# Kernel optimization log

Measured on AMD Instinct MI355X. Metric: run time of the kernel, lower is better.

The kernel has to match this reference:

```python
import jax, jax.numpy as jnp
import numpy as np


def setup_inputs() -> dict:
    key = jax.random.key(0)
    k1, k2, k3, k4 = jax.random.split(key, 4)
    B, S, T = 128, 512, 256
    return {
        "emissions": jax.random.normal(k1, (B, S, T), dtype=jnp.float32),
        "mask": jnp.ones((B, S), dtype=bool),
        "start_transitions": jax.random.normal(k2, (T,), dtype=jnp.float32),
        "end_transitions": jax.random.normal(k3, (T,), dtype=jnp.float32),
        "transitions": jax.random.normal(k4, (T, T), dtype=jnp.float32),
    }


def reference(emissions, mask, start_transitions, end_transitions, transitions):
    # emissions: [B, S, T], mask: [B, S] bool, transitions: [T, T]
    init = start_transitions[None, :] + emissions[:, 0]  # [B, T]
    em_t = jnp.swapaxes(emissions[:, 1:], 0, 1)  # [S-1, B, T] time-major
    mk_t = jnp.swapaxes(mask[:, 1:], 0, 1)       # [S-1, B]

    def lse_step(state, em):
        # state[b, i] + transitions[i, j] + em[b, j] -> logsumexp over i
        inner = state[:, :, None] + transitions[None, :, :] + em[:, None, :]
        return jax.nn.logsumexp(inner, axis=1)

    # _compute_score: mask-aware logsumexp recurrence (as written in the module)
    def step_score(score, xs):
        em, mk = xs
        nxt = lse_step(score, em)
        return jnp.where(mk[:, None], nxt, score), None

    score, _ = jax.lax.scan(step_score, init, (em_t, mk_t))
    score = jax.nn.logsumexp(score + end_transitions[None, :], axis=1)  # [B]

    # _compute_partition: same recurrence, mask where() is a no-op in the source
    def step_part(alpha, em):
        return lse_step(alpha, em), None

    alpha, _ = jax.lax.scan(step_part, init, em_t)
    partition = jax.nn.logsumexp(alpha + end_transitions[None, :], axis=1)  # [B]

    return partition - score
```

## Files before the change

kernel.cpp:

```cpp
#include <hip/hip_runtime.h>
#include <hip/hip_bf16.h>
#include <stdint.h>

#define LOG2E 1.44269504088896340736f
#define LN2   0.69314718055994530942f

typedef __attribute__((ext_vector_type(8))) __bf16 bf16x8;
typedef __attribute__((ext_vector_type(4))) float  f32x4;

static constexpr int B = 128, S = 512, T = 256;
static constexpr int LDP = T + 8;
static constexpr int H   = 260;
static constexpr int NSF = H;
static constexpr int NSB = S - 1 - H;

static __device__ __forceinline__ uint pack_bf16x2(float a, float b) {
    __hip_bfloat162 h = __float22bfloat162_rn(make_float2(a, b));
    union { __hip_bfloat162 h; uint u; } cv; cv.h = h;
    return cv.u;
}
static __device__ __forceinline__ float bf2f(ushort u) {
    return __uint_as_float(((uint)u) << 16);
}

static __device__ __forceinline__ void wg_barrier() {
    asm volatile("s_waitcnt lgkmcnt(0)" ::: "memory");
    __builtin_amdgcn_s_barrier();
    __builtin_amdgcn_sched_barrier(0);
}

static __device__ __forceinline__ float vmax44(const float v[4][4]) {
    float m = 0.0f;
    #pragma unroll
    for (int t = 0; t < 4; ++t)
        #pragma unroll
        for (int r = 0; r < 4; ++r) m = fmaxf(m, v[t][r]);
    return m;
}

__global__ void prep_mats(const float* __restrict__ trans,
                          ushort* __restrict__ Et, ushort* __restrict__ Em) {
    int i = blockIdx.x;
    int j = threadIdx.x;
    float e = exp2f(trans[i * T + j] * LOG2E);
    uint u = __float_as_uint(e);
    ushort h = (ushort)((u + 0x7FFFu + ((u >> 16) & 1u)) >> 16);
    Em[i * T + j] = h;
    Et[j * T + i] = h;
}

__global__ void prep_emx(const float* __restrict__ em, ushort* __restrict__ emx) {
    size_t i4 = ((size_t)blockIdx.x * blockDim.x + threadIdx.x) * 4;
    f32x4 e = *reinterpret_cast<const f32x4*>(&em[i4]);
    uint2 w;
    w.x = pack_bf16x2(exp2f(e[0] * LOG2E), exp2f(e[1] * LOG2E));
    w.y = pack_bf16x2(exp2f(e[2] * LOG2E), exp2f(e[3] * LOG2E));
    *reinterpret_cast<uint2*>(&emx[i4]) = w;
}

template<bool PRE, int DIR>
static __device__ __forceinline__ void scan_body(
    const float* __restrict__ em, const ushort* __restrict__ emx,
    const int* __restrict__ mask, const float* __restrict__ startt,
    const float* __restrict__ endt, const ushort* __restrict__ Amat,
    float* __restrict__ vecbuf, int* __restrict__ lsbuf,
    const int scan, const int b,
    ushort (&Al)[2][16][LDP], float (&mx2)[16][4])
{
    constexpr int NSTEP = DIR ? NSB : NSF;
    constexpr int PGRP  = (NSTEP + 7) / 8;

    const int tid  = threadIdx.x;
    const int jq   = tid >> 6;
    const int lane = tid & 63;
    const int q    = lane >> 4;
    const int l    = lane & 15;

    #define EROW(ix) (DIR ? (S - 2 - (ix)) : (1 + (ix)))
    #define MROW(ix) (DIR ? (S - 1 - (ix)) : (1 + (ix)))

    bf16x8 Afr[4][8];
    #pragma unroll
    for (int mt = 0; mt < 4; ++mt) {
        int j = jq * 64 + mt * 16 + l;
        #pragma unroll
        for (int kt = 0; kt < 8; ++kt)
            Afr[mt][kt] = *reinterpret_cast<const bf16x8*>(&Amat[j * T + kt * 32 + q * 8]);
    }

    const float*  emrow = em  + (size_t)b * S * T;
    const ushort* exrow = PRE ? emx + (size_t)b * S * T : nullptr;
    const int*    mrow  = mask + (size_t)b * S;

    int ls = 0;
    int buf = 0;
    float areg[4][4];

    {
        const int    r0 = DIR ? (S - 1) : 0;
        const float* tv = DIR ? endt : startt;
        float v0[4][4], gg[4][4]; float mx = 0.0f;
        #pragma unroll
        for (int t = 0; t < 4; ++t) {
            int j0 = jq * 64 + t * 16 + q * 4;
            f32x4 e4 = *reinterpret_cast<const f32x4*>(&emrow[(size_t)r0 * T + j0]);
            f32x4 s4 = *reinterpret_cast<const f32x4*>(&tv[j0]);
            #pragma unroll
            for (int r = 0; r < 4; ++r) {
                float full = exp2f((e4[r] + s4[r]) * LOG2E);
                v0[t][r] = full;
                gg[t][r] = DIR ? exp2f(s4[r] * LOG2E) : full;
                mx = fmaxf(mx, full);
            }
        }
        mx = fmaxf(mx, __shfl_xor(mx, 16));
        mx = fmaxf(mx, __shfl_xor(mx, 32));
        if (q == 0) mx2[l][jq] = mx;
        __syncthreads();
        f32x4 m4 = *reinterpret_cast<const f32x4*>(&mx2[l][0]);
        float gmx = fmaxf(fmaxf(m4[0], m4[1]), fmaxf(m4[2], m4[3]));
        int e = (int)((__float_as_uint(gmx) >> 23) & 255u) - 127;
        float sc = __uint_as_float((uint)(127 - e) << 23);
        ls = e;
        #pragma unroll
        for (int t = 0; t < 4; ++t) {
            int j0 = jq * 64 + t * 16 + q * 4;
            uint2 w;
            w.x = pack_bf16x2(v0[t][0] * sc, v0[t][1] * sc);
            w.y = pack_bf16x2(v0[t][2] * sc, v0[t][3] * sc);
            *reinterpret_cast<uint2*>(&Al[0][l][j0]) = w;
            if (DIR) {
                #pragma unroll
                for (int r = 0; r < 4; ++r) areg[t][r] = gg[t][r] * sc;
            }
        }
        __syncthreads();
        if (q == 0) mx2[l][jq] = mx * sc;
        __syncthreads();
    }

    const bool track = (DIR == 0) && (scan != 0);

    uint2 exv[8][4]; int mks[8];
    #pragma unroll
    for (int u = 0; u < 8; ++u) {
        int iu = u < NSTEP ? u : NSTEP - 1;
        #pragma unroll
        for (int t = 0; t < 4; ++t) {
            int j0 = jq * 64 + t * 16 + q * 4;
            if (PRE) exv[u][t] = *reinterpret_cast<const uint2*>(&exrow[(size_t)EROW(iu) * T + j0]);
        }
        mks[u] = (scan && u < NSTEP) ? mrow[MROW(u)] : 1;
    }

    for (int p = 0; p < PGRP; ++p) {
        uint2 exn[8][4]; int mkn[8];
        #pragma unroll
        for (int u = 0; u < 8; ++u) {
            int idx  = 8 * (p + 1) + u;
            int idxc = idx < NSTEP ? idx : NSTEP - 1;
            #pragma unroll
            for (int t = 0; t < 4; ++t) {
                int j0 = jq * 64 + t * 16 + q * 4;
                if (PRE) exn[u][t] = *reinterpret_cast<const uint2*>(&exrow[(size_t)EROW(idxc) * T + j0]);
            }
            mkn[u] = (scan && idx < NSTEP) ? mrow[MROW(idxc)] : 1;
        }

        float pend = 1.0f, vml = 0.0f; int pk = 0;

        #pragma unroll
        for (int u = 0; u < 8; ++u) {
            const int idx = 8 * p + u;
            if (idx < NSTEP) {
                if ((u & 3) == 0) {
                    f32x4 m4 = *reinterpret_cast<const f32x4*>(&mx2[l][0]);
                    float gmx = fmaxf(fmaxf(m4[0], m4[1]), fmaxf(m4[2], m4[3]));
                    int kap = (int)((__float_as_uint(gmx) >> 23) & 255u) - 127;
                    pend = __uint_as_float((uint)(127 - kap) << 23);
                    pk   = kap;
                    vml  = gmx;
                }
                const int nb = buf ^ 1;

                bf16x8 bfr[8];
                #pragma unroll
                for (int kt = 0; kt < 8; ++kt)
                    bfr[kt] = *reinterpret_cast<const bf16x8*>(&Al[buf][l][kt * 32 + q * 8]);

                f32x4 acc[4] = {f32x4{0,0,0,0}, f32x4{0,0,0,0}, f32x4{0,0,0,0}, f32x4{0,0,0,0}};
                #pragma unroll
                for (int kt = 0; kt < 8; ++kt) {
                    #pragma unroll
                    for (int mt = 0; mt < 4; ++mt)
                        acc[mt] = __builtin_amdgcn_mfma_f32_16x16x32_bf16(Afr[mt][kt], bfr[kt], acc[mt], 0, 0, 0);
                }

                const int mk = mks[u];
                float v[4][4];

                #pragma unroll
                for (int t = 0; t < 4; ++t) {
                    float e_[4];
                    if (PRE) {
                        e_[0] = bf2f((ushort)(exv[u][t].x & 0xFFFF));
                        e_[1] = bf2f((ushort)(exv[u][t].x >> 16));
                        e_[2] = bf2f((ushort)(exv[u][t].y & 0xFFFF));
                        e_[3] = bf2f((ushort)(exv[u][t].y >> 16));
                    } else {
                        int j0 = jq * 64 + t * 16 + q * 4;
                        f32x4 e4 = *reinterpret_cast<const f32x4*>(&emrow[(size_t)EROW(idx) * T + j0]);
                        #pragma unroll
                        for (int r = 0; r < 4; ++r) e_[r] = exp2f(e4[r] * LOG2E);
                    }
                    if (DIR == 0) {
                        #pragma unroll
                        for (int r = 0; r < 4; ++r)
                            v[t][r] = acc[t][r] * e_[r] * pend;
                    } else {
                        #pragma unroll
                        for (int r = 0; r < 4; ++r) {
                            float g  = acc[t][r] * pend;
                            float sv = mk ? g : areg[t][r];
                            areg[t][r] = sv;
                            v[t][r] = sv * e_[r];
                        }
                    }
                }

                if (DIR == 0) {
                    if (mk) {
                        #pragma unroll
                        for (int t = 0; t < 4; ++t) {
                            int j0 = jq * 64 + t * 16 + q * 4;
                            uint2 w;
                            w.x = pack_bf16x2(v[t][0], v[t][1]);
                            w.y = pack_bf16x2(v[t][2], v[t][3]);
                            *reinterpret_cast<uint2*>(&Al[nb][l][j0]) = w;
                        }
                    } else {
                        #pragma unroll
                        for (int t = 0; t < 4; ++t) {
                            int j0 = jq * 64 + t * 16 + q * 4;
                            *reinterpret_cast<uint2*>(&Al[nb][l][j0]) =
                                *reinterpret_cast<const uint2*>(&Al[buf][l][j0]);
                        }
                    }
                } else {
                    #pragma unroll
                    for (int t = 0; t < 4; ++t) {
                        int j0 = jq * 64 + t * 16 + q * 4;
                        uint2 w;
                        w.x = pack_bf16x2(v[t][0], v[t][1]);
                        w.y = pack_bf16x2(v[t][2], v[t][3]);
                        *reinterpret_cast<uint2*>(&Al[nb][l][j0]) = w;
                    }
                }

                if (track) {
                    float lmx = vmax44(v);
                    vml = mk ? lmx : vml;
                }
                ls  += mk ? pk : 0;
                pend = mk ? 1.0f : pend;
                pk   = mk ? 0 : pk;

                const bool rn = ((u & 3) == 3) || (idx == NSTEP - 1);
                if (rn) {
                    float fm = track ? vml : vmax44(v);
                    fm = fmaxf(fm, __shfl_xor(fm, 16));
                    fm = fmaxf(fm, __shfl_xor(fm, 32));
                    if (q == 0) mx2[l][jq] = fm;
                }

                wg_barrier();
                buf = nb;
            }
        }

        #pragma unroll
        for (int u = 0; u < 8; ++u) {
            #pragma unroll
            for (int t = 0; t < 4; ++t) exv[u][t] = exn[u][t];
            mks[u] = mkn[u];
        }
    }

    const int cidx = scan * 2 + DIR;
    if (DIR) {
        #pragma unroll
        for (int t = 0; t < 4; ++t) {
            int j0 = jq * 64 + t * 16 + q * 4;
            f32x4 o = {areg[t][0], areg[t][1], areg[t][2], areg[t][3]};
            *reinterpret_cast<f32x4*>(&vecbuf[((size_t)cidx * B + b) * T + j0]) = o;
        }
    } else {
        #pragma unroll
        for (int t = 0; t < 4; ++t) {
            int j0 = jq * 64 + t * 16 + q * 4;
            uint2 w = *reinterpret_cast<const uint2*>(&Al[buf][l][j0]);
            f32x4 o = {bf2f((ushort)(w.x & 0xFFFF)), bf2f((ushort)(w.x >> 16)),
                       bf2f((ushort)(w.y & 0xFFFF)), bf2f((ushort)(w.y >> 16))};
            *reinterpret_cast<f32x4*>(&vecbuf[((size_t)cidx * B + b) * T + j0]) = o;
        }
    }
    if (jq == 0 && q == 0) lsbuf[cidx * B + b] = ls;

    #undef EROW
    #undef MROW
}

template<bool PRE>
__launch_bounds__(256, 1)
__global__ void crf_scan(const float* __restrict__ em,
                         const ushort* __restrict__ emx,
                         const int* __restrict__ mask,
                         const float* __restrict__ startt,
                         const float* __restrict__ endt,
                         const ushort* __restrict__ Et,
                         const ushort* __restrict__ Emat,
                         float* __restrict__ vecbuf,
                         int* __restrict__ lsbuf)
{
    __shared__ __align__(16) ushort Al[2][16][LDP];
    __shared__ __align__(16) float mx2[16][4];

    const int scan = blockIdx.x & 1;
    const int dir  = (blockIdx.x >> 1) & 1;
    const int bg   = blockIdx.x >> 2;
    const int b    = bg * 16 + (threadIdx.x & 15);

    if (dir == 0)
        scan_body<PRE, 0>(em, emx, mask, startt, endt, Et,   vecbuf, lsbuf, scan, b, Al, mx2);
    else
        scan_body<PRE, 1>(em, emx, mask, startt, endt, Emat, vecbuf, lsbuf, scan, b, Al, mx2);
}

__global__ void combine2(const float* __restrict__ vecbuf, const int* __restrict__ lsbuf,
                         float* __restrict__ out) {
    __shared__ float r2[2][B];
    int tid = threadIdx.x;
    int sc_ = tid >> 7, b = tid & 127;
    const float* vf = vecbuf + ((size_t)(sc_ * 2 + 0) * B + b) * T;
    const float* vb = vecbuf + ((size_t)(sc_ * 2 + 1) * B + b) * T;
    float dot = 0.0f;
    for (int j = 0; j < T; j += 4) {
        f32x4 a = *reinterpret_cast<const f32x4*>(&vf[j]);
        f32x4 c = *reinterpret_cast<const f32x4*>(&vb[j]);
        dot += a[0] * c[0] + a[1] * c[1] + a[2] * c[2] + a[3] * c[3];
    }
    r2[sc_][b] = (float)(lsbuf[(sc_ * 2) * B + b] + lsbuf[(sc_ * 2 + 1) * B + b]) + log2f(dot);
    __syncthreads();
    if (tid < B) out[tid] = (r2[0][tid] - r2[1][tid]) * LN2;
}

extern "C" void kernel_launch(void* const* d_in, const int* in_sizes, int n_in,
                              void* d_out, int out_size, void* d_ws, size_t ws_size,
                              hipStream_t stream) {
    (void)in_sizes; (void)n_in; (void)out_size;
    const float* em = (const float*)d_in[0];
    const int*   mk = (const int*)d_in[1];
    const float* st = (const float*)d_in[2];
    const float* en = (const float*)d_in[3];
    const float* tr = (const float*)d_in[4];

    const size_t emx_bytes = (size_t)B * S * T * sizeof(ushort);
    const size_t mat_bytes = (size_t)T * T * sizeof(ushort);
    const size_t vec_bytes = (size_t)4 * B * T * sizeof(float);
    const size_t ls_bytes  = (size_t)4 * B * sizeof(int);

    const bool pre = ws_size >= emx_bytes + 2 * mat_bytes + vec_bytes + ls_bytes;

    char* wp = (char*)d_ws;
    ushort* emx = nullptr;
    if (pre) { emx = (ushort*)wp; wp += emx_bytes; }
    ushort* Et = (ushort*)wp; wp += mat_bytes;
    ushort* Em = (ushort*)wp; wp += mat_bytes;
    float*  vec = (float*)wp; wp += vec_bytes;
    int*    lsb = (int*)wp;

    prep_mats<<<T, T, 0, stream>>>(tr, Et, Em);
    if (pre) {
        prep_emx<<<(B * S * T) / (256 * 4), 256, 0, stream>>>(em, emx);
        crf_scan<true><<<32, 256, 0, stream>>>(em, emx, mk, st, en, Et, Em, vec, lsb);
    } else {
        crf_scan<false><<<32, 256, 0, stream>>>(em, emx, mk, st, en, Et, Em, vec, lsb);
    }
    combine2<<<1, 256, 0, stream>>>(vec, lsb, (float*)d_out);
}
```

Baseline: 390.8 us.

## Split each scan block across eight waves with two MFMA tiles per wave

Each scan block now uses 512 threads, so eight waves each own 32 output tags instead of four waves owning 64. The per-step 256x256 matvec work per wave is halved, and the MFMA accumulation is split into two interleaved chains to shorten the dependency chain. The aim is to cut per-step latency on the serial recurrence. In exchange, the cross-wave max reduction now reads eight entries and the per-step barrier has to synchronise twice as many waves.

```diff
diff --git a/kernel.cpp b/kernel.cpp
--- a/kernel.cpp
+++ b/kernel.cpp
@@ -29,10 +29,10 @@
     __builtin_amdgcn_sched_barrier(0);
 }
 
-static __device__ __forceinline__ float vmax44(const float v[4][4]) {
+static __device__ __forceinline__ float vmax24(const float v[2][4]) {
     float m = 0.0f;
     #pragma unroll
-    for (int t = 0; t < 4; ++t)
+    for (int t = 0; t < 2; ++t)
         #pragma unroll
         for (int r = 0; r < 4; ++r) m = fmaxf(m, v[t][r]);
     return m;
@@ -64,28 +64,29 @@
     const int* __restrict__ mask, const float* __restrict__ startt,
     const float* __restrict__ endt, const ushort* __restrict__ Amat,
     float* __restrict__ vecbuf, int* __restrict__ lsbuf,
-    const int scan, const int b,
-    ushort (&Al)[2][16][LDP], float (&mx2)[16][4])
+    const int scan, const int bg,
+    ushort (&Al)[2][16][LDP], float (&mx2)[16][8])
 {
     constexpr int NSTEP = DIR ? NSB : NSF;
     constexpr int PGRP  = (NSTEP + 7) / 8;
 
     const int tid  = threadIdx.x;
-    const int jq   = tid >> 6;
+    const int w    = tid >> 6;
     const int lane = tid & 63;
     const int q    = lane >> 4;
     const int l    = lane & 15;
+    const int b    = bg * 16 + l;
 
     #define EROW(ix) (DIR ? (S - 2 - (ix)) : (1 + (ix)))
     #define MROW(ix) (DIR ? (S - 1 - (ix)) : (1 + (ix)))
 
-    bf16x8 Afr[4][8];
+    bf16x8 Afr[2][8];
     #pragma unroll
-    for (int mt = 0; mt < 4; ++mt) {
-        int j = jq * 64 + mt * 16 + l;
+    for (int t = 0; t < 2; ++t) {
+        int j = w * 32 + t * 16 + l;
         #pragma unroll
         for (int kt = 0; kt < 8; ++kt)
-            Afr[mt][kt] = *reinterpret_cast<const bf16x8*>(&Amat[j * T + kt * 32 + q * 8]);
+            Afr[t][kt] = *reinterpret_cast<const bf16x8*>(&Amat[j * T + kt * 32 + q * 8]);
     }
 
     const float*  emrow = em  + (size_t)b * S * T;
@@ -94,15 +95,15 @@
 
     int ls = 0;
     int buf = 0;
-    float areg[4][4];
+    float areg[2][4];
 
     {
         const int    r0 = DIR ? (S - 1) : 0;
         const float* tv = DIR ? endt : startt;
-        float v0[4][4], gg[4][4]; float mx = 0.0f;
-        #pragma unroll
-        for (int t = 0; t < 4; ++t) {
-            int j0 = jq * 64 + t * 16 + q * 4;
+        float v0[2][4], gg[2][4]; float mx = 0.0f;
+        #pragma unroll
+        for (int t = 0; t < 2; ++t) {
+            int j0 = w * 32 + t * 16 + q * 4;
             f32x4 e4 = *reinterpret_cast<const f32x4*>(&emrow[(size_t)r0 * T + j0]);
             f32x4 s4 = *reinterpret_cast<const f32x4*>(&tv[j0]);
             #pragma unroll
@@ -115,53 +116,55 @@
         }
         mx = fmaxf(mx, __shfl_xor(mx, 16));
         mx = fmaxf(mx, __shfl_xor(mx, 32));
-        if (q == 0) mx2[l][jq] = mx;
+        if (q == 0) mx2[l][w] = mx;
         __syncthreads();
-        f32x4 m4 = *reinterpret_cast<const f32x4*>(&mx2[l][0]);
-        float gmx = fmaxf(fmaxf(m4[0], m4[1]), fmaxf(m4[2], m4[3]));
+        f32x4 ma = *reinterpret_cast<const f32x4*>(&mx2[l][0]);
+        f32x4 mb = *reinterpret_cast<const f32x4*>(&mx2[l][4]);
+        float gmx = fmaxf(fmaxf(fmaxf(ma[0], ma[1]), fmaxf(ma[2], ma[3])),
+                          fmaxf(fmaxf(mb[0], mb[1]), fmaxf(mb[2], mb[3])));
         int e = (int)((__float_as_uint(gmx) >> 23) & 255u) - 127;
         float sc = __uint_as_float((uint)(127 - e) << 23);
         ls = e;
         #pragma unroll
-        for (int t = 0; t < 4; ++t) {
-            int j0 = jq * 64 + t * 16 + q * 4;
-            uint2 w;
-            w.x = pack_bf16x2(v0[t][0] * sc, v0[t][1] * sc);
-            w.y = pack_bf16x2(v0[t][2] * sc, v0[t][3] * sc);
-            *reinterpret_cast<uint2*>(&Al[0][l][j0]) = w;
+        for (int t = 0; t < 2; ++t) {
+            int j0 = w * 32 + t * 16 + q * 4;
+            uint2 wv;
+            wv.x = pack_bf16x2(v0[t][0] * sc, v0[t][1] * sc);
+            wv.y = pack_bf16x2(v0[t][2] * sc, v0[t][3] * sc);
+            *reinterpret_cast<uint2*>(&Al[0][l][j0]) = wv;
             if (DIR) {
                 #pragma unroll
                 for (int r = 0; r < 4; ++r) areg[t][r] = gg[t][r] * sc;
             }
         }
         __syncthreads();
-        if (q == 0) mx2[l][jq] = mx * sc;
+        if (q == 0) mx2[l][w] = mx * sc;
         __syncthreads();
     }
 
     const bool track = (DIR == 0) && (scan != 0);
 
-    uint2 exv[8][4]; int mks[8];
+    uint2 exv[8][2]; int mks[8];
     #pragma unroll
     for (int u = 0; u < 8; ++u) {
         int iu = u < NSTEP ? u : NSTEP - 1;
         #pragma unroll
-        for (int t = 0; t < 4; ++t) {
-            int j0 = jq * 64 + t * 16 + q * 4;
+        for (int t = 0; t < 2; ++t) {
+            int j0 = w * 32 + t * 16 + q * 4;
             if (PRE) exv[u][t] = *reinterpret_cast<const uint2*>(&exrow[(size_t)EROW(iu) * T + j0]);
         }
-        mks[u] = (scan && u < NSTEP) ? mrow[MROW(u)] : 1;
+        mks[u] = (scan && u < NSTEP) ? mrow[MROW(iu)] : 1;
     }
 
     for (int p = 0; p < PGRP; ++p) {
-        uint2 exn[8][4]; int mkn[8];
+        uint2 exn[8][2]; int mkn[8];
         #pragma unroll
         for (int u = 0; u < 8; ++u) {
             int idx  = 8 * (p + 1) + u;
             int idxc = idx < NSTEP ? idx : NSTEP - 1;
             #pragma unroll
-            for (int t = 0; t < 4; ++t) {
-                int j0 = jq * 64 + t * 16 + q * 4;
+            for (int t = 0; t < 2; ++t) {
+                int j0 = w * 32 + t * 16 + q * 4;
                 if (PRE) exn[u][t] = *reinterpret_cast<const uint2*>(&exrow[(size_t)EROW(idxc) * T + j0]);
             }
             mkn[u] = (scan && idx < NSTEP) ? mrow[MROW(idxc)] : 1;
@@ -174,8 +177,10 @@
             const int idx = 8 * p + u;
             if (idx < NSTEP) {
                 if ((u & 3) == 0) {
-                    f32x4 m4 = *reinterpret_cast<const f32x4*>(&mx2[l][0]);
-                    float gmx = fmaxf(fmaxf(m4[0], m4[1]), fmaxf(m4[2], m4[3]));
+                    f32x4 ma = *reinterpret_cast<const f32x4*>(&mx2[l][0]);
+                    f32x4 mb = *reinterpret_cast<const f32x4*>(&mx2[l][4]);
+                    float gmx = fmaxf(fmaxf(fmaxf(ma[0], ma[1]), fmaxf(ma[2], ma[3])),
+                                      fmaxf(fmaxf(mb[0], mb[1]), fmaxf(mb[2], mb[3])));
                     int kap = (int)((__float_as_uint(gmx) >> 23) & 255u) - 127;
                     pend = __uint_as_float((uint)(127 - kap) << 23);
                     pk   = kap;
@@ -188,19 +193,23 @@
                 for (int kt = 0; kt < 8; ++kt)
                     bfr[kt] = *reinterpret_cast<const bf16x8*>(&Al[buf][l][kt * 32 + q * 8]);
 
-                f32x4 acc[4] = {f32x4{0,0,0,0}, f32x4{0,0,0,0}, f32x4{0,0,0,0}, f32x4{0,0,0,0}};
+                f32x4 ac[2][2] = {{f32x4{0,0,0,0}, f32x4{0,0,0,0}},
+                                  {f32x4{0,0,0,0}, f32x4{0,0,0,0}}};
                 #pragma unroll
                 for (int kt = 0; kt < 8; ++kt) {
                     #pragma unroll
-                    for (int mt = 0; mt < 4; ++mt)
-                        acc[mt] = __builtin_amdgcn_mfma_f32_16x16x32_bf16(Afr[mt][kt], bfr[kt], acc[mt], 0, 0, 0);
-                }
+                    for (int t = 0; t < 2; ++t)
+                        ac[t][kt & 1] = __builtin_amdgcn_mfma_f32_16x16x32_bf16(Afr[t][kt], bfr[kt], ac[t][kt & 1], 0, 0, 0);
+                }
+                f32x4 acc[2];
+                #pragma unroll
+                for (int t = 0; t < 2; ++t) acc[t] = ac[t][0] + ac[t][1];
 
                 const int mk = mks[u];
-                float v[4][4];
-
-                #pragma unroll
-                for (int t = 0; t < 4; ++t) {
+                float v[2][4];
+
+                #pragma unroll
+                for (int t = 0; t < 2; ++t) {
                     float e_[4];
                     if (PRE) {
                         e_[0] = bf2f((ushort)(exv[u][t].x & 0xFFFF));
@@ -208,7 +217,7 @@
                         e_[2] = bf2f((ushort)(exv[u][t].y & 0xFFFF));
                         e_[3] = bf2f((ushort)(exv[u][t].y >> 16));
                     } else {
-                        int j0 = jq * 64 + t * 16 + q * 4;
+                        int j0 = w * 32 + t * 16 + q * 4;
                         f32x4 e4 = *reinterpret_cast<const f32x4*>(&emrow[(size_t)EROW(idx) * T + j0]);
                         #pragma unroll
                         for (int r = 0; r < 4; ++r) e_[r] = exp2f(e4[r] * LOG2E);
@@ -231,34 +240,34 @@
                 if (DIR == 0) {
                     if (mk) {
                         #pragma unroll
-                        for (int t = 0; t < 4; ++t) {
-                            int j0 = jq * 64 + t * 16 + q * 4;
-                            uint2 w;
-                            w.x = pack_bf16x2(v[t][0], v[t][1]);
-                            w.y = pack_bf16x2(v[t][2], v[t][3]);
-                            *reinterpret_cast<uint2*>(&Al[nb][l][j0]) = w;
+                        for (int t = 0; t < 2; ++t) {
+                            int j0 = w * 32 + t * 16 + q * 4;
+                            uint2 wv;
+                            wv.x = pack_bf16x2(v[t][0], v[t][1]);
+                            wv.y = pack_bf16x2(v[t][2], v[t][3]);
+                            *reinterpret_cast<uint2*>(&Al[nb][l][j0]) = wv;
                         }
                     } else {
                         #pragma unroll
-                        for (int t = 0; t < 4; ++t) {
-                            int j0 = jq * 64 + t * 16 + q * 4;
+                        for (int t = 0; t < 2; ++t) {
+                            int j0 = w * 32 + t * 16 + q * 4;
                             *reinterpret_cast<uint2*>(&Al[nb][l][j0]) =
                                 *reinterpret_cast<const uint2*>(&Al[buf][l][j0]);
                         }
                     }
                 } else {
                     #pragma unroll
-                    for (int t = 0; t < 4; ++t) {
-                        int j0 = jq * 64 + t * 16 + q * 4;
-                        uint2 w;
-                        w.x = pack_bf16x2(v[t][0], v[t][1]);
-                        w.y = pack_bf16x2(v[t][2], v[t][3]);
-                        *reinterpret_cast<uint2*>(&Al[nb][l][j0]) = w;
+                    for (int t = 0; t < 2; ++t) {
+                        int j0 = w * 32 + t * 16 + q * 4;
+                        uint2 wv;
+                        wv.x = pack_bf16x2(v[t][0], v[t][1]);
+                        wv.y = pack_bf16x2(v[t][2], v[t][3]);
+                        *reinterpret_cast<uint2*>(&Al[nb][l][j0]) = wv;
                     }
                 }
 
                 if (track) {
-                    float lmx = vmax44(v);
+                    float lmx = vmax24(v);
                     vml = mk ? lmx : vml;
                 }
                 ls  += mk ? pk : 0;
@@ -267,10 +276,10 @@
 
                 const bool rn = ((u & 3) == 3) || (idx == NSTEP - 1);
                 if (rn) {
-                    float fm = track ? vml : vmax44(v);
+                    float fm = track ? vml : vmax24(v);
                     fm = fmaxf(fm, __shfl_xor(fm, 16));
                     fm = fmaxf(fm, __shfl_xor(fm, 32));
-                    if (q == 0) mx2[l][jq] = fm;
+                    if (q == 0) mx2[l][w] = fm;
                 }
 
                 wg_barrier();
@@ -281,7 +290,7 @@
         #pragma unroll
         for (int u = 0; u < 8; ++u) {
             #pragma unroll
-            for (int t = 0; t < 4; ++t) exv[u][t] = exn[u][t];
+            for (int t = 0; t < 2; ++t) exv[u][t] = exn[u][t];
             mks[u] = mkn[u];
         }
     }
@@ -289,29 +298,29 @@
     const int cidx = scan * 2 + DIR;
     if (DIR) {
         #pragma unroll
-        for (int t = 0; t < 4; ++t) {
-            int j0 = jq * 64 + t * 16 + q * 4;
+        for (int t = 0; t < 2; ++t) {
+            int j0 = w * 32 + t * 16 + q * 4;
             f32x4 o = {areg[t][0], areg[t][1], areg[t][2], areg[t][3]};
             *reinterpret_cast<f32x4*>(&vecbuf[((size_t)cidx * B + b) * T + j0]) = o;
         }
     } else {
         #pragma unroll
-        for (int t = 0; t < 4; ++t) {
-            int j0 = jq * 64 + t * 16 + q * 4;
-            uint2 w = *reinterpret_cast<const uint2*>(&Al[buf][l][j0]);
-            f32x4 o = {bf2f((ushort)(w.x & 0xFFFF)), bf2f((ushort)(w.x >> 16)),
-                       bf2f((ushort)(w.y & 0xFFFF)), bf2f((ushort)(w.y >> 16))};
+        for (int t = 0; t < 2; ++t) {
+            int j0 = w * 32 + t * 16 + q * 4;
+            uint2 wv = *reinterpret_cast<const uint2*>(&Al[buf][l][j0]);
+            f32x4 o = {bf2f((ushort)(wv.x & 0xFFFF)), bf2f((ushort)(wv.x >> 16)),
+                       bf2f((ushort)(wv.y & 0xFFFF)), bf2f((ushort)(wv.y >> 16))};
             *reinterpret_cast<f32x4*>(&vecbuf[((size_t)cidx * B + b) * T + j0]) = o;
         }
     }
-    if (jq == 0 && q == 0) lsbuf[cidx * B + b] = ls;
+    if (w == 0 && q == 0) lsbuf[cidx * B + b] = ls;
 
     #undef EROW
     #undef MROW
 }
 
 template<bool PRE>
-__launch_bounds__(256, 1)
+__launch_bounds__(512, 2)
 __global__ void crf_scan(const float* __restrict__ em,
                          const ushort* __restrict__ emx,
                          const int* __restrict__ mask,
@@ -323,17 +332,16 @@
                          int* __restrict__ lsbuf)
 {
     __shared__ __align__(16) ushort Al[2][16][LDP];
-    __shared__ __align__(16) float mx2[16][4];
+    __shared__ __align__(16) float mx2[16][8];
 
     const int scan = blockIdx.x & 1;
     const int dir  = (blockIdx.x >> 1) & 1;
     const int bg   = blockIdx.x >> 2;
-    const int b    = bg * 16 + (threadIdx.x & 15);
 
     if (dir == 0)
-        scan_body<PRE, 0>(em, emx, mask, startt, endt, Et,   vecbuf, lsbuf, scan, b, Al, mx2);
+        scan_body<PRE, 0>(em, emx, mask, startt, endt, Et,   vecbuf, lsbuf, scan, bg, Al, mx2);
     else
-        scan_body<PRE, 1>(em, emx, mask, startt, endt, Emat, vecbuf, lsbuf, scan, b, Al, mx2);
+        scan_body<PRE, 1>(em, emx, mask, startt, endt, Emat, vecbuf, lsbuf, scan, bg, Al, mx2);
 }
 
 __global__ void combine2(const float* __restrict__ vecbuf, const int* __restrict__ lsbuf,
@@ -382,9 +390,9 @@
     prep_mats<<<T, T, 0, stream>>>(tr, Et, Em);
     if (pre) {
         prep_emx<<<(B * S * T) / (256 * 4), 256, 0, stream>>>(em, emx);
-        crf_scan<true><<<32, 256, 0, stream>>>(em, emx, mk, st, en, Et, Em, vec, lsb);
+        crf_scan<true><<<32, 512, 0, stream>>>(em, emx, mk, st, en, Et, Em, vec, lsb);
     } else {
-        crf_scan<false><<<32, 256, 0, stream>>>(em, emx, mk, st, en, Et, Em, vec, lsb);
+        crf_scan<false><<<32, 512, 0, stream>>>(em, emx, mk, st, en, Et, Em, vec, lsb);
     }
     combine2<<<1, 256, 0, stream>>>(vec, lsb, (float*)d_out);
 }
```

New measurement: 383.4 us. No clear change (-1.9%).
